# Performance work log

Hardware: AMD Instinct MI355X
Metric: run time of the kernel (lower is better)

Reference implementation:

```python
import jax, jax.numpy as jnp
import numpy as np

B, C, N, T = 16, 32, 1024, 64
C_OUT = 32
ORDER = 2
SMOOTH_DEPTH = 1


def setup_inputs() -> dict:
    key = jax.random.key(0)
    k1, k2, k3, k4 = jax.random.split(key, 4)
    x = jax.random.normal(k1, (B, C, N, T), dtype=jnp.float32)
    # row-normalized dense adjacencies (transition matrices), as used in Graph-WaveNet-style supports
    AL = jax.random.uniform(k2, (N, N), dtype=jnp.float32)
    AL = AL / AL.sum(axis=-1, keepdims=True)
    AS_pos = jax.random.uniform(k3, (N, N), dtype=jnp.float32)
    AS_pos = AS_pos / AS_pos.sum(axis=-1, keepdims=True)
    # 1x1 conv mlp: in_channels = (order*support_len+1)*c_in = 3*C, out_channels = C_OUT
    W_mlp = jax.random.normal(k4, (C_OUT, (ORDER + 1) * C), dtype=jnp.float32) * 0.02
    b_mlp = jnp.zeros((C_OUT,), dtype=jnp.float32)
    return {"x": x, "AL": AL, "AS_pos": AS_pos, "W_mlp": W_mlp, "b_mlp": b_mlp}


def reference(x, AL, AS_pos, W_mlp, b_mlp):
    # gcn_module.forward with short_bool=True, smooth_depth=SMOOTH_DEPTH, eval mode (no dropout)
    ALp = jnp.linalg.matrix_power(AL, SMOOTH_DEPTH)          # [N,N]
    # torch.einsum('bckj,ik->bcij', x, ALp): contract node dim of x against ALp
    x_long = jnp.einsum('ik,bckt->bcit', ALp, x)             # [B,C,N,T]
    x_short = x - x_long
    outs = [x]
    for _ in range(ORDER):
        # dnconv: einsum('nvw,ncwl->ncvl', A, x) with 2D A broadcast over batch
        x_long = jnp.einsum('vw,bcwt->bcvt', AL, x_long)
        x_short = jnp.einsum('vw,bcwt->bcvt', AS_pos, x_short)
        outs.append(x_long + x_short)
    h = jnp.concatenate(outs, axis=1)                        # [B,(ORDER+1)*C,N,T]
    # 1x1 conv == channel mixing
    h = jnp.einsum('oc,bcnt->bont', W_mlp, h) + b_mlp[None, :, None, None]
    return h
```

## Files before the change

kernel.cpp:

```cpp
#include <hip/hip_runtime.h>


typedef __bf16 bf16x8 __attribute__((ext_vector_type(8)));
typedef float f32x4 __attribute__((ext_vector_type(4)));
typedef unsigned int u32x4 __attribute__((ext_vector_type(4)));
typedef unsigned int u32x2 __attribute__((ext_vector_type(2)));

__device__ __forceinline__ unsigned short f2bf(float f) {
  unsigned u = __builtin_bit_cast(unsigned, f);
  u += 0x7fffu + ((u >> 16) & 1u);
  return (unsigned short)(u >> 16);
}
__device__ __forceinline__ float bf2f(unsigned short h) {
  unsigned u = ((unsigned)h) << 16;
  return __builtin_bit_cast(float, u);
}

static constexpr size_t OFF_YC    = 0;
static constexpr size_t OFF_ALBF  = 201326592;
static constexpr size_t OFF_ALT   = OFF_ALBF  + 2097152;
static constexpr size_t OFF_ASBF  = OFF_ALT   + 2097152;
static constexpr size_t OFF_AST   = OFF_ASBF  + 2097152;
static constexpr size_t OFF_AL2   = OFF_AST   + 2097152;
static constexpr size_t OFF_AL2T  = OFF_AL2   + 2097152;
static constexpr size_t OFF_ASAL  = OFF_AL2T  + 2097152;
static constexpr size_t OFF_AS2   = OFF_ASAL  + 2097152;
static constexpr size_t OFF_AL3   = OFF_AS2   + 2097152;
static constexpr size_t OFF_AS2AL = OFF_AL3   + 2097152;
static constexpr size_t OFF_G     = OFF_AS2AL + 2097152;

__global__ __launch_bounds__(256) void k_prep(const float* __restrict__ AL,
                                              const float* __restrict__ AS,
                                              unsigned short* __restrict__ ALn,
                                              unsigned short* __restrict__ ALtr,
                                              unsigned short* __restrict__ ASn,
                                              unsigned short* __restrict__ AStr) {
  const float* src = blockIdx.z ? AS : AL;
  unsigned short* dstN = blockIdx.z ? ASn : ALn;
  unsigned short* dstT = blockIdx.z ? AStr : ALtr;
  __shared__ float Xs[64][65];
  const int tid = threadIdx.x;
  const int r0 = blockIdx.x * 64, c0 = blockIdx.y * 64;
  const int lrow = tid >> 4, lc4 = tid & 15;
#pragma unroll
  for (int rr = 0; rr < 4; rr++) {
    int row = rr * 16 + lrow;
    float4 v = *(const float4*)(src + (size_t)(r0 + row) * 1024 + c0 + lc4 * 4);
    Xs[row][lc4 * 4 + 0] = v.x;
    Xs[row][lc4 * 4 + 1] = v.y;
    Xs[row][lc4 * 4 + 2] = v.z;
    Xs[row][lc4 * 4 + 3] = v.w;
    unsigned lo = (unsigned)f2bf(v.x) | ((unsigned)f2bf(v.y) << 16);
    unsigned hi = (unsigned)f2bf(v.z) | ((unsigned)f2bf(v.w) << 16);
    u32x2 pk = {lo, hi};
    *(u32x2*)(dstN + (size_t)(r0 + row) * 1024 + c0 + lc4 * 4) = pk;
  }
  __syncthreads();
  const int wc = tid & 7;
#pragma unroll
  for (int u = 0; u < 2; u++) {
    int t = u * 32 + (tid >> 3);
    unsigned v0 = (unsigned)f2bf(Xs[wc * 8 + 0][t]) | ((unsigned)f2bf(Xs[wc * 8 + 1][t]) << 16);
    unsigned v1 = (unsigned)f2bf(Xs[wc * 8 + 2][t]) | ((unsigned)f2bf(Xs[wc * 8 + 3][t]) << 16);
    unsigned v2 = (unsigned)f2bf(Xs[wc * 8 + 4][t]) | ((unsigned)f2bf(Xs[wc * 8 + 5][t]) << 16);
    unsigned v3 = (unsigned)f2bf(Xs[wc * 8 + 6][t]) | ((unsigned)f2bf(Xs[wc * 8 + 7][t]) << 16);
    u32x4 pk = {v0, v1, v2, v3};
    *(u32x4*)(dstT + (size_t)(c0 + t) * 1024 + r0 + wc * 8) = pk;
  }
}

__device__ __forceinline__ void gemm128_bt(const unsigned short* __restrict__ A,
                                           const unsigned short* __restrict__ Bt,
                                           unsigned short* __restrict__ Cp,
                                           int K, size_t ldc, int m0, int n0) {
  __shared__ unsigned short As[128 * 32];
  __shared__ unsigned short Bs[128 * 32];
  const int tid = threadIdx.x;
  const int wave = tid >> 6, lane = tid & 63;
  const int lane15 = lane & 15, quad = lane >> 4;
  const int wm = wave & 1, wn = wave >> 1;
  const int srow = lane >> 2;
  const int schunk = (lane & 3) * 8;

  const unsigned short* gA0 = A + (size_t)(m0 + wave * 16 + srow) * K + schunk;
  const unsigned short* gA1 = A + (size_t)(m0 + 64 + wave * 16 + srow) * K + schunk;
  const unsigned short* gB0 = Bt + (size_t)(n0 + wave * 16 + srow) * K + schunk;
  const unsigned short* gB1 = Bt + (size_t)(n0 + 64 + wave * 16 + srow) * K + schunk;
  unsigned short* lA0 = As + (wave * 16) * 32;
  unsigned short* lA1 = As + (64 + wave * 16) * 32;
  unsigned short* lB0 = Bs + (wave * 16) * 32;
  unsigned short* lB1 = Bs + (64 + wave * 16) * 32;

  f32x4 acc[4][4];
#pragma unroll
  for (int i = 0; i < 4; i++)
#pragma unroll
    for (int j = 0; j < 4; j++) acc[i][j] = (f32x4){0.f, 0.f, 0.f, 0.f};

  const unsigned short* pa = As + (wm * 64 + lane15) * 32 + quad * 8;
  const unsigned short* pb = Bs + (wn * 64 + lane15) * 32 + quad * 8;

  for (int kb = 0; kb < K; kb += 32) {
    __syncthreads();
    __builtin_amdgcn_global_load_lds(
        (const __attribute__((address_space(1))) unsigned int*)(gA0 + kb),
        (__attribute__((address_space(3))) unsigned int*)lA0, 16, 0, 0);
    __builtin_amdgcn_global_load_lds(
        (const __attribute__((address_space(1))) unsigned int*)(gA1 + kb),
        (__attribute__((address_space(3))) unsigned int*)lA1, 16, 0, 0);
    __builtin_amdgcn_global_load_lds(
        (const __attribute__((address_space(1))) unsigned int*)(gB0 + kb),
        (__attribute__((address_space(3))) unsigned int*)lB0, 16, 0, 0);
    __builtin_amdgcn_global_load_lds(
        (const __attribute__((address_space(1))) unsigned int*)(gB1 + kb),
        (__attribute__((address_space(3))) unsigned int*)lB1, 16, 0, 0);
    __syncthreads();

    bf16x8 av[4], bv[4];
#pragma unroll
    for (int mt = 0; mt < 4; mt++) av[mt] = *(const bf16x8*)(pa + mt * 16 * 32);
#pragma unroll
    for (int nt = 0; nt < 4; nt++) bv[nt] = *(const bf16x8*)(pb + nt * 16 * 32);
#pragma unroll
    for (int mt = 0; mt < 4; mt++)
#pragma unroll
      for (int nt = 0; nt < 4; nt++)
        acc[mt][nt] = __builtin_amdgcn_mfma_f32_16x16x32_bf16(av[mt], bv[nt], acc[mt][nt], 0, 0, 0);
  }

#pragma unroll
  for (int mt = 0; mt < 4; mt++) {
#pragma unroll
    for (int nt = 0; nt < 4; nt++) {
      const int col = n0 + wn * 64 + nt * 16 + lane15;
#pragma unroll
      for (int r = 0; r < 4; r++) {
        const int row = m0 + wm * 64 + mt * 16 + quad * 4 + r;
        Cp[(size_t)row * ldc + col] = f2bf(acc[mt][nt][r]);
      }
    }
  }
}

__global__ __launch_bounds__(256) void k_gemm_pre(char* ws, int stage) {
  const unsigned short* A;
  const unsigned short* Bt;
  unsigned short* Cp;
  const int z = blockIdx.z;
  unsigned short* ALbf = (unsigned short*)(ws + OFF_ALBF);
  unsigned short* ALt  = (unsigned short*)(ws + OFF_ALT);
  unsigned short* ASbf = (unsigned short*)(ws + OFF_ASBF);
  unsigned short* ASt  = (unsigned short*)(ws + OFF_AST);
  unsigned short* AL2  = (unsigned short*)(ws + OFF_AL2);
  unsigned short* ASAL = (unsigned short*)(ws + OFF_ASAL);
  unsigned short* AS2  = (unsigned short*)(ws + OFF_AS2);
  unsigned short* AL3  = (unsigned short*)(ws + OFF_AL3);
  unsigned short* AS2AL= (unsigned short*)(ws + OFF_AS2AL);
  if (stage == 0) {
    if (z == 0)      { A = ALbf; Bt = ALt;  Cp = AL2;  }
    else if (z == 1) { A = ASbf; Bt = ALt;  Cp = ASAL; }
    else             { A = ASbf; Bt = ASt;  Cp = AS2;  }
  } else {
    if (z == 0)      { A = AL2;  Bt = ALt;  Cp = AL3;  }
    else             { A = AS2;  Bt = ALt;  Cp = AS2AL;}
  }
  gemm128_bt(A, Bt, Cp, 1024, 1024, blockIdx.y * 128, blockIdx.x * 128);
}

__global__ __launch_bounds__(256) void k_assemble_G(const unsigned short* __restrict__ AL2,
                                                    const unsigned short* __restrict__ ASAL,
                                                    const float* __restrict__ ASf,
                                                    const unsigned short* __restrict__ AL3,
                                                    const unsigned short* __restrict__ AS2,
                                                    const unsigned short* __restrict__ AS2AL,
                                                    const float* __restrict__ W,
                                                    unsigned short* __restrict__ Wall,
                                                    unsigned short* __restrict__ G) {
  if (blockIdx.x == 0) {
    for (int k = threadIdx.x; k < 3072; k += 256) {
      int oo = k >> 5, c = k & 31;
      Wall[k] = f2bf(W[(oo & 31) * 96 + (oo >> 5) * 32 + c]);
    }
  }
  int i = blockIdx.x * 256 + threadIdx.x;
  int r = i >> 10, c = i & 1023;
  float g1 = bf2f(AL2[i]) + ASf[i] - bf2f(ASAL[i]);
  float g2 = bf2f(AL3[i]) + bf2f(AS2[i]) - bf2f(AS2AL[i]);
  G[(size_t)r * 2048 + c]        = f2bf(g1);
  G[(size_t)r * 2048 + 1024 + c] = f2bf(g2);
}

__global__ __launch_bounds__(256, 8) void k_mix_g(const float* __restrict__ x,
                                                  const unsigned short* __restrict__ Wall,
                                                  unsigned short* __restrict__ Yc) {
  const int tid = threadIdx.x;
  const int sid = (blockIdx.x & 7) * 256 + (blockIdx.x >> 3);
  const int b   = sid >> 7;
  const int n8g = sid & 127;
  const int nbase = n8g * 8;
  const int wave = tid >> 6, lane = tid & 63;
  const int lane15 = lane & 15, quad = lane >> 4;
  const int t = wave * 16 + lane15;

  bf16x8 afr[6];
#pragma unroll
  for (int ot = 0; ot < 6; ot++)
    afr[ot] = *(const bf16x8*)(Wall + (ot * 16 + lane15) * 32 + quad * 8);

  const float* xb = x + (size_t)b * 2097152 + (size_t)(quad * 8) * 65536 + t;

  bf16x8 bfr[8];
#pragma unroll
  for (int nl = 0; nl < 8; nl++) {
    const float* xp = xb + (size_t)(nbase + nl) * 64;
    unsigned u[4];
#pragma unroll
    for (int e = 0; e < 4; e++) {
      float a  = xp[(size_t)(2 * e) * 65536];
      float c2 = xp[(size_t)(2 * e + 1) * 65536];
      u[e] = (unsigned)f2bf(a) | ((unsigned)f2bf(c2) << 16);
    }
    u32x4 pk = {u[0], u[1], u[2], u[3]};
    bfr[nl] = __builtin_bit_cast(bf16x8, pk);
  }

#pragma unroll
  for (int ot = 0; ot < 6; ot++) {
    f32x4 acc[8];
    const f32x4 z = (f32x4){0.f, 0.f, 0.f, 0.f};
#pragma unroll
    for (int nl = 0; nl < 8; nl++)
      acc[nl] = __builtin_amdgcn_mfma_f32_16x16x32_bf16(afr[ot], bfr[nl], z, 0, 0, 0);
    const int og = ot >> 1;
    const int o  = (ot & 1) * 16 + quad * 4;
    const size_t plane = (size_t)(og * 128 + n8g) * 262144;
#pragma unroll
    for (int r = 0; r < 4; r++) {
      unsigned u0 = (unsigned)f2bf(acc[0][r]) | ((unsigned)f2bf(acc[1][r]) << 16);
      unsigned u1 = (unsigned)f2bf(acc[2][r]) | ((unsigned)f2bf(acc[3][r]) << 16);
      unsigned u2 = (unsigned)f2bf(acc[4][r]) | ((unsigned)f2bf(acc[5][r]) << 16);
      unsigned u3 = (unsigned)f2bf(acc[6][r]) | ((unsigned)f2bf(acc[7][r]) << 16);
      u32x4 pk = {u0, u1, u2, u3};
      size_t j = (size_t)(b * 32 + o + r) * 64 + t;
      *(u32x4*)(Yc + plane + j * 8) = pk;
    }
  }
}

__global__ __launch_bounds__(512) void k_gemm_main8(const unsigned short* __restrict__ A,
                                                    const unsigned short* __restrict__ Yc,
                                                    const float* __restrict__ bm,
                                                    float* __restrict__ out) {
  __shared__ unsigned short lds[65536];
  const int tid = threadIdx.x;
  const int wave = tid >> 6, lane = tid & 63;
  const int lane15 = lane & 15, quad = lane >> 4;
  const int wr = wave >> 2, wc = wave & 3;

  const int bid = blockIdx.x;
  const int swz = (bid & 7) * 64 + (bid >> 3);
  const int nx = swz >> 2, my = swz & 3;
  const int m0 = my * 256, n0 = nx * 256;

  const int srow = tid >> 3;
  const int cB   = (tid & 7) ^ (srow & 7);
  const int skc  = cB << 3;
  const int ldst0 = (tid & ~63) << 3;

#define STAGE_A(rowbase, ldsptr, ktile)                                                 \
  do {                                                                                  \
    const unsigned short* _g =                                                          \
        A + (size_t)((rowbase) + srow) * 2048 + (size_t)((ktile) * 64 + skc);           \
    __builtin_amdgcn_global_load_lds(                                                   \
        (const __attribute__((address_space(1))) unsigned int*)_g,                      \
        (__attribute__((address_space(3))) unsigned int*)((ldsptr) + ldst0), 16, 0, 0); \
    __builtin_amdgcn_global_load_lds(                                                   \
        (const __attribute__((address_space(1))) unsigned int*)(_g + 131072),           \
        (__attribute__((address_space(3))) unsigned int*)((ldsptr) + 4096 + ldst0),     \
        16, 0, 0);                                                                      \
  } while (0)

#define STAGE_B(rowbase, ldsptr, ktile)                                                 \
  do {                                                                                  \
    const unsigned short* _g = Yc + (size_t)(128 + (ktile) * 8 + cB) * 262144 +         \
                               (size_t)((rowbase) + srow) * 8;                          \
    __builtin_amdgcn_global_load_lds(                                                   \
        (const __attribute__((address_space(1))) unsigned int*)_g,                      \
        (__attribute__((address_space(3))) unsigned int*)((ldsptr) + ldst0), 16, 0, 0); \
    __builtin_amdgcn_global_load_lds(                                                   \
        (const __attribute__((address_space(1))) unsigned int*)(_g + 512),              \
        (__attribute__((address_space(3))) unsigned int*)((ldsptr) + 4096 + ldst0),     \
        16, 0, 0);                                                                      \
  } while (0)

#define RD_BFR()                                                                        \
  _Pragma("unroll") for (int n = 0; n < 4; n++)                                         \
      _Pragma("unroll") for (int kk = 0; kk < 2; kk++)                                  \
          bfr[n][kk] = *(const bf16x8*)(pB + n * 1024 + aks[kk]);

#define RD_AFR(mA, mB)                                                                  \
  _Pragma("unroll") for (int kk = 0; kk < 2; kk++) {                                    \
    afr[0][kk] = *(const bf16x8*)(pA + (mA) * 1024 + aks[kk]);                          \
    afr[1][kk] = *(const bf16x8*)(pA + (mB) * 1024 + aks[kk]);                          \
  }

#define MFMA2(i0)                                                                       \
  _Pragma("unroll") for (int kk = 0; kk < 2; kk++)                                      \
      _Pragma("unroll") for (int mi = 0; mi < 2; mi++)                                  \
          _Pragma("unroll") for (int n = 0; n < 4; n++)                                 \
              acc[(i0) + mi][n] = __builtin_amdgcn_mfma_f32_16x16x32_bf16(              \
                  afr[mi][kk], bfr[n][kk], acc[(i0) + mi][n], 0, 0, 0);

#define BAR()   asm volatile("" ::: "memory"); __builtin_amdgcn_s_barrier();
#define LGKM0() asm volatile("s_waitcnt lgkmcnt(0)" ::: "memory");                      \
                __builtin_amdgcn_sched_barrier(0);
#define LGKM8() asm volatile("s_waitcnt lgkmcnt(8)" ::: "memory");
#define PRIO1() __builtin_amdgcn_s_setprio(1);
#define PRIO0() __builtin_amdgcn_s_setprio(0);

  unsigned short* Acur = lds;
  unsigned short* Bcur = lds + 16384;
  unsigned short* Aalt = lds + 32768;
  unsigned short* Balt = lds + 49152;

  f32x4 acc[8][4];
#pragma unroll
  for (int i = 0; i < 8; i++)
#pragma unroll
    for (int j = 0; j < 4; j++) acc[i][j] = (f32x4){0.f, 0.f, 0.f, 0.f};

  const int swz8 = (lane15 & 7) << 3;
  int aks[2];
  aks[0] = (quad << 3) ^ swz8;
  aks[1] = (32 | (quad << 3)) ^ swz8;

  bf16x8 bfr[4][2], afr[2][2];

  STAGE_A(m0,       Acur,        0);
  STAGE_A(m0 + 128, Acur + 8192, 0);
  STAGE_B(n0,       Bcur,        0);
  STAGE_B(n0 + 128, Bcur + 8192, 0);
  STAGE_B(n0,       Balt,        1);
  STAGE_B(n0 + 128, Balt + 8192, 1);
  asm volatile("s_waitcnt vmcnt(4)" ::: "memory");
  BAR();

  for (int t = 0; t < 30; ++t) {
    const unsigned short* pA = Acur + (wr * 128 + lane15) * 64;
    const unsigned short* pB = Bcur + (wc * 64 + lane15) * 64;
    RD_BFR();
    RD_AFR(0, 1);
    STAGE_A(m0, Aalt, t + 1);
    LGKM8();
    BAR(); LGKM0();
    PRIO1(); MFMA2(0); PRIO0();
    BAR();
    RD_AFR(2, 3);
    STAGE_A(m0 + 128, Aalt + 8192, t + 1);
    BAR(); LGKM0();
    PRIO1(); MFMA2(2); PRIO0();
    BAR();
    RD_AFR(4, 5);
    STAGE_B(n0, Bcur, t + 2);
    BAR(); LGKM0();
    PRIO1(); MFMA2(4); PRIO0();
    BAR();
    RD_AFR(6, 7);
    STAGE_B(n0 + 128, Bcur + 8192, t + 2);
    BAR(); LGKM0();
    PRIO1(); MFMA2(6); PRIO0();
    asm volatile("s_waitcnt vmcnt(4)" ::: "memory");
    BAR();
    unsigned short* tmp;
    tmp = Acur; Acur = Aalt; Aalt = tmp;
    tmp = Bcur; Bcur = Balt; Balt = tmp;
  }

  {
    const unsigned short* pA = Acur + (wr * 128 + lane15) * 64;
    const unsigned short* pB = Bcur + (wc * 64 + lane15) * 64;
    RD_BFR();
    RD_AFR(0, 1);
    STAGE_A(m0, Aalt, 31);
    LGKM8();
    BAR(); LGKM0();
    PRIO1(); MFMA2(0); PRIO0();
    BAR();
    RD_AFR(2, 3);
    STAGE_A(m0 + 128, Aalt + 8192, 31);
    BAR(); LGKM0();
    PRIO1(); MFMA2(2); PRIO0();
    BAR();
    RD_AFR(4, 5);
    BAR(); LGKM0();
    PRIO1(); MFMA2(4); PRIO0();
    BAR();
    RD_AFR(6, 7);
    BAR(); LGKM0();
    PRIO1(); MFMA2(6); PRIO0();
    asm volatile("s_waitcnt vmcnt(0)" ::: "memory");
    BAR();
    unsigned short* tmp;
    tmp = Acur; Acur = Aalt; Aalt = tmp;
    tmp = Bcur; Bcur = Balt; Balt = tmp;
  }

  {
    const unsigned short* pA = Acur + (wr * 128 + lane15) * 64;
    const unsigned short* pB = Bcur + (wc * 64 + lane15) * 64;
    RD_BFR();
#pragma unroll
    for (int p = 0; p < 4; p++) {
      RD_AFR(2 * p, 2 * p + 1);
      LGKM0();
      MFMA2(2 * p);
    }
  }

#pragma unroll
  for (int mt = 0; mt < 8; mt++) {
    const int row = m0 + wr * 128 + mt * 16 + quad * 4;
#pragma unroll
    for (int nf = 0; nf < 4; nf++) {
      const int col = n0 + wc * 64 + nf * 16 + lane15;
      const int bo_idx = col >> 6;
      const float bo = bm[bo_idx & 31];
      const size_t obase = (size_t)bo_idx * 65536 + (col & 63);
      ushort4 yv = *(const ushort4*)(Yc + (size_t)(row >> 3) * 262144 +
                                     (size_t)col * 8 + (row & 7));
      out[obase + (size_t)(row + 0) * 64] = acc[mt][nf][0] + bf2f(yv.x) + bo;
      out[obase + (size_t)(row + 1) * 64] = acc[mt][nf][1] + bf2f(yv.y) + bo;
      out[obase + (size_t)(row + 2) * 64] = acc[mt][nf][2] + bf2f(yv.z) + bo;
      out[obase + (size_t)(row + 3) * 64] = acc[mt][nf][3] + bf2f(yv.w) + bo;
    }
  }
#undef STAGE_A
#undef STAGE_B
#undef RD_BFR
#undef RD_AFR
#undef MFMA2
#undef BAR
#undef LGKM0
#undef LGKM8
#undef PRIO1
#undef PRIO0
}

extern "C" void kernel_launch(void* const* d_in, const int* in_sizes, int n_in,
                              void* d_out, int out_size, void* d_ws, size_t ws_size,
                              hipStream_t stream) {
  const float* x  = (const float*)d_in[0];
  const float* AL = (const float*)d_in[1];
  const float* AS = (const float*)d_in[2];
  const float* W  = (const float*)d_in[3];
  const float* bm = (const float*)d_in[4];
  float* out = (float*)d_out;
  char* ws = (char*)d_ws;

  unsigned short* Yc    = (unsigned short*)(ws + OFF_YC);
  unsigned short* ALbf  = (unsigned short*)(ws + OFF_ALBF);
  unsigned short* ALt   = (unsigned short*)(ws + OFF_ALT);
  unsigned short* ASbf  = (unsigned short*)(ws + OFF_ASBF);
  unsigned short* ASt   = (unsigned short*)(ws + OFF_AST);
  unsigned short* AL2   = (unsigned short*)(ws + OFF_AL2);
  unsigned short* ASAL  = (unsigned short*)(ws + OFF_ASAL);
  unsigned short* AS2   = (unsigned short*)(ws + OFF_AS2);
  unsigned short* AL3   = (unsigned short*)(ws + OFF_AL3);
  unsigned short* AS2AL = (unsigned short*)(ws + OFF_AS2AL);
  unsigned short* Gm    = (unsigned short*)(ws + OFF_G);
  unsigned short* Wall  = (unsigned short*)(ws + OFF_ALBF);

  k_prep<<<dim3(16, 16, 2), 256, 0, stream>>>(AL, AS, ALbf, ALt, ASbf, ASt);
  k_gemm_pre<<<dim3(8, 8, 3), 256, 0, stream>>>(ws, 0);
  k_gemm_pre<<<dim3(8, 8, 2), 256, 0, stream>>>(ws, 1);
  k_assemble_G<<<4096, 256, 0, stream>>>(AL2, ASAL, AS, AL3, AS2, AS2AL, W, Wall, Gm);
  k_mix_g<<<2048, 256, 0, stream>>>(x, Wall, Yc);
  k_gemm_main8<<<dim3(512, 1, 1), 512, 0, stream>>>(Gm, Yc, bm, out);
}
```

Before: 511.2 us.

## Halve main GEMM K-tile to 32 to cut LDS and raise occupancy

```diff
diff --git a/kernel.cpp b/kernel.cpp
--- a/kernel.cpp
+++ b/kernel.cpp
@@ -247,11 +247,11 @@
   }
 }
 
-__global__ __launch_bounds__(512) void k_gemm_main8(const unsigned short* __restrict__ A,
-                                                    const unsigned short* __restrict__ Yc,
-                                                    const float* __restrict__ bm,
-                                                    float* __restrict__ out) {
-  __shared__ unsigned short lds[65536];
+__global__ __launch_bounds__(512, 4) void k_gemm_main8(const unsigned short* __restrict__ A,
+                                                       const unsigned short* __restrict__ Yc,
+                                                       const float* __restrict__ bm,
+                                                       float* __restrict__ out) {
+  __shared__ unsigned short lds[32768];
   const int tid = threadIdx.x;
   const int wave = tid >> 6, lane = tid & 63;
   const int lane15 = lane & 15, quad = lane >> 4;
@@ -262,66 +262,52 @@
   const int nx = swz >> 2, my = swz & 3;
   const int m0 = my * 256, n0 = nx * 256;
 
-  const int srow = tid >> 3;
-  const int cB   = (tid & 7) ^ (srow & 7);
-  const int skc  = cB << 3;
-  const int ldst0 = (tid & ~63) << 3;
-
-#define STAGE_A(rowbase, ldsptr, ktile)                                                 \
-  do {                                                                                  \
-    const unsigned short* _g =                                                          \
-        A + (size_t)((rowbase) + srow) * 2048 + (size_t)((ktile) * 64 + skc);           \
-    __builtin_amdgcn_global_load_lds(                                                   \
-        (const __attribute__((address_space(1))) unsigned int*)_g,                      \
-        (__attribute__((address_space(3))) unsigned int*)((ldsptr) + ldst0), 16, 0, 0); \
-    __builtin_amdgcn_global_load_lds(                                                   \
-        (const __attribute__((address_space(1))) unsigned int*)(_g + 131072),           \
-        (__attribute__((address_space(3))) unsigned int*)((ldsptr) + 4096 + ldst0),     \
-        16, 0, 0);                                                                      \
+  const int srow = tid >> 2;
+  const int cswz = (tid & 3) ^ (srow & 3);
+  const int ldst0 = tid * 8;
+
+#define STAGE_A32(rowbase, dsthalf, ktile)                                              \
+  do {                                                                                 \
+    const unsigned short* _g =                                                         \
+        A + (size_t)((rowbase) + srow) * 2048 + (size_t)((ktile) * 32 + cswz * 8);     \
+    __builtin_amdgcn_global_load_lds(                                                  \
+        (const __attribute__((address_space(1))) unsigned int*)_g,                     \
+        (__attribute__((address_space(3))) unsigned int*)((dsthalf) + ldst0), 16, 0, 0);\
   } while (0)
 
-#define STAGE_B(rowbase, ldsptr, ktile)                                                 \
-  do {                                                                                  \
-    const unsigned short* _g = Yc + (size_t)(128 + (ktile) * 8 + cB) * 262144 +         \
-                               (size_t)((rowbase) + srow) * 8;                          \
-    __builtin_amdgcn_global_load_lds(                                                   \
-        (const __attribute__((address_space(1))) unsigned int*)_g,                      \
-        (__attribute__((address_space(3))) unsigned int*)((ldsptr) + ldst0), 16, 0, 0); \
-    __builtin_amdgcn_global_load_lds(                                                   \
-        (const __attribute__((address_space(1))) unsigned int*)(_g + 512),              \
-        (__attribute__((address_space(3))) unsigned int*)((ldsptr) + 4096 + ldst0),     \
-        16, 0, 0);                                                                      \
+#define STAGE_B32(rowbase, dsthalf, ktile)                                              \
+  do {                                                                                 \
+    const unsigned short* _g = Yc + (size_t)(128 + (ktile) * 4 + cswz) * 262144 +      \
+                               (size_t)((rowbase) + srow) * 8;                         \
+    __builtin_amdgcn_global_load_lds(                                                  \
+        (const __attribute__((address_space(1))) unsigned int*)_g,                     \
+        (__attribute__((address_space(3))) unsigned int*)((dsthalf) + ldst0), 16, 0, 0);\
   } while (0)
 
-#define RD_BFR()                                                                        \
+#define RD_B32()                                                                        \
   _Pragma("unroll") for (int n = 0; n < 4; n++)                                         \
-      _Pragma("unroll") for (int kk = 0; kk < 2; kk++)                                  \
-          bfr[n][kk] = *(const bf16x8*)(pB + n * 1024 + aks[kk]);
-
-#define RD_AFR(mA, mB)                                                                  \
-  _Pragma("unroll") for (int kk = 0; kk < 2; kk++) {                                    \
-    afr[0][kk] = *(const bf16x8*)(pA + (mA) * 1024 + aks[kk]);                          \
-    afr[1][kk] = *(const bf16x8*)(pA + (mB) * 1024 + aks[kk]);                          \
-  }
-
-#define MFMA2(i0)                                                                       \
-  _Pragma("unroll") for (int kk = 0; kk < 2; kk++)                                      \
-      _Pragma("unroll") for (int mi = 0; mi < 2; mi++)                                  \
-          _Pragma("unroll") for (int n = 0; n < 4; n++)                                 \
-              acc[(i0) + mi][n] = __builtin_amdgcn_mfma_f32_16x16x32_bf16(              \
-                  afr[mi][kk], bfr[n][kk], acc[(i0) + mi][n], 0, 0, 0);
+      bfr[n] = *(const bf16x8*)(pB + n * 512 + aks);
+
+#define RD_A32(m0i)                                                                     \
+  _Pragma("unroll") for (int mi = 0; mi < 4; mi++)                                      \
+      afr[mi] = *(const bf16x8*)(pA + ((m0i) + mi) * 512 + aks);
+
+#define MFMA16(i0)                                                                      \
+  _Pragma("unroll") for (int mi = 0; mi < 4; mi++)                                      \
+      _Pragma("unroll") for (int n = 0; n < 4; n++)                                     \
+          acc[(i0) + mi][n] = __builtin_amdgcn_mfma_f32_16x16x32_bf16(                  \
+              afr[mi], bfr[n], acc[(i0) + mi][n], 0, 0, 0);
 
 #define BAR()   asm volatile("" ::: "memory"); __builtin_amdgcn_s_barrier();
 #define LGKM0() asm volatile("s_waitcnt lgkmcnt(0)" ::: "memory");                      \
                 __builtin_amdgcn_sched_barrier(0);
-#define LGKM8() asm volatile("s_waitcnt lgkmcnt(8)" ::: "memory");
 #define PRIO1() __builtin_amdgcn_s_setprio(1);
 #define PRIO0() __builtin_amdgcn_s_setprio(0);
 
   unsigned short* Acur = lds;
-  unsigned short* Bcur = lds + 16384;
-  unsigned short* Aalt = lds + 32768;
-  unsigned short* Balt = lds + 49152;
+  unsigned short* Bcur = lds + 8192;
+  unsigned short* Aalt = lds + 16384;
+  unsigned short* Balt = lds + 24576;
 
   f32x4 acc[8][4];
 #pragma unroll
@@ -329,47 +315,35 @@
 #pragma unroll
     for (int j = 0; j < 4; j++) acc[i][j] = (f32x4){0.f, 0.f, 0.f, 0.f};
 
-  const int swz8 = (lane15 & 7) << 3;
-  int aks[2];
-  aks[0] = (quad << 3) ^ swz8;
-  aks[1] = (32 | (quad << 3)) ^ swz8;
-
-  bf16x8 bfr[4][2], afr[2][2];
-
-  STAGE_A(m0,       Acur,        0);
-  STAGE_A(m0 + 128, Acur + 8192, 0);
-  STAGE_B(n0,       Bcur,        0);
-  STAGE_B(n0 + 128, Bcur + 8192, 0);
-  STAGE_B(n0,       Balt,        1);
-  STAGE_B(n0 + 128, Balt + 8192, 1);
-  asm volatile("s_waitcnt vmcnt(4)" ::: "memory");
+  const int aks = ((quad ^ (lane15 & 3)) << 3);
+
+  bf16x8 bfr[4], afr[4];
+
+  STAGE_A32(m0,       Acur,        0);
+  STAGE_A32(m0 + 128, Acur + 4096, 0);
+  STAGE_B32(n0,       Bcur,        0);
+  STAGE_B32(n0 + 128, Bcur + 4096, 0);
+  STAGE_B32(n0,       Balt,        1);
+  STAGE_B32(n0 + 128, Balt + 4096, 1);
+  asm volatile("s_waitcnt vmcnt(2)" ::: "memory");
   BAR();
 
-  for (int t = 0; t < 30; ++t) {
-    const unsigned short* pA = Acur + (wr * 128 + lane15) * 64;
-    const unsigned short* pB = Bcur + (wc * 64 + lane15) * 64;
-    RD_BFR();
-    RD_AFR(0, 1);
-    STAGE_A(m0, Aalt, t + 1);
-    LGKM8();
+  for (int t = 0; t < 62; ++t) {
+    const unsigned short* pA = Acur + wr * 4096 + lane15 * 32;
+    const unsigned short* pB = Bcur + (wc >> 1) * 4096 + ((wc & 1) * 64 + lane15) * 32;
+    RD_B32();
+    RD_A32(0);
+    STAGE_A32(m0,       Aalt,        t + 1);
+    STAGE_A32(m0 + 128, Aalt + 4096, t + 1);
     BAR(); LGKM0();
-    PRIO1(); MFMA2(0); PRIO0();
+    PRIO1(); MFMA16(0); PRIO0();
     BAR();
-    RD_AFR(2, 3);
-    STAGE_A(m0 + 128, Aalt + 8192, t + 1);
+    RD_A32(4);
+    STAGE_B32(n0,       Bcur,        t + 2);
+    STAGE_B32(n0 + 128, Bcur + 4096, t + 2);
     BAR(); LGKM0();
-    PRIO1(); MFMA2(2); PRIO0();
-    BAR();
-    RD_AFR(4, 5);
-    STAGE_B(n0, Bcur, t + 2);
-    BAR(); LGKM0();
-    PRIO1(); MFMA2(4); PRIO0();
-    BAR();
-    RD_AFR(6, 7);
-    STAGE_B(n0 + 128, Bcur + 8192, t + 2);
-    BAR(); LGKM0();
-    PRIO1(); MFMA2(6); PRIO0();
-    asm volatile("s_waitcnt vmcnt(4)" ::: "memory");
+    PRIO1(); MFMA16(4); PRIO0();
+    asm volatile("s_waitcnt vmcnt(2)" ::: "memory");
     BAR();
     unsigned short* tmp;
     tmp = Acur; Acur = Aalt; Aalt = tmp;
@@ -377,27 +351,18 @@
   }
 
   {
-    const unsigned short* pA = Acur + (wr * 128 + lane15) * 64;
-    const unsigned short* pB = Bcur + (wc * 64 + lane15) * 64;
-    RD_BFR();
-    RD_AFR(0, 1);
-    STAGE_A(m0, Aalt, 31);
-    LGKM8();
+    const unsigned short* pA = Acur + wr * 4096 + lane15 * 32;
+    const unsigned short* pB = Bcur + (wc >> 1) * 4096 + ((wc & 1) * 64 + lane15) * 32;
+    RD_B32();
+    RD_A32(0);
+    STAGE_A32(m0,       Aalt,        63);
+    STAGE_A32(m0 + 128, Aalt + 4096, 63);
     BAR(); LGKM0();
-    PRIO1(); MFMA2(0); PRIO0();
+    PRIO1(); MFMA16(0); PRIO0();
     BAR();
-    RD_AFR(2, 3);
-    STAGE_A(m0 + 128, Aalt + 8192, 31);
+    RD_A32(4);
     BAR(); LGKM0();
-    PRIO1(); MFMA2(2); PRIO0();
-    BAR();
-    RD_AFR(4, 5);
-    BAR(); LGKM0();
-    PRIO1(); MFMA2(4); PRIO0();
-    BAR();
-    RD_AFR(6, 7);
-    BAR(); LGKM0();
-    PRIO1(); MFMA2(6); PRIO0();
+    PRIO1(); MFMA16(4); PRIO0();
     asm volatile("s_waitcnt vmcnt(0)" ::: "memory");
     BAR();
     unsigned short* tmp;
@@ -406,15 +371,15 @@
   }
 
   {
-    const unsigned short* pA = Acur + (wr * 128 + lane15) * 64;
-    const unsigned short* pB = Bcur + (wc * 64 + lane15) * 64;
-    RD_BFR();
-#pragma unroll
-    for (int p = 0; p < 4; p++) {
-      RD_AFR(2 * p, 2 * p + 1);
-      LGKM0();
-      MFMA2(2 * p);
-    }
+    const unsigned short* pA = Acur + wr * 4096 + lane15 * 32;
+    const unsigned short* pB = Bcur + (wc >> 1) * 4096 + ((wc & 1) * 64 + lane15) * 32;
+    RD_B32();
+    RD_A32(0);
+    LGKM0();
+    MFMA16(0);
+    RD_A32(4);
+    LGKM0();
+    MFMA16(4);
   }
 
 #pragma unroll
@@ -434,14 +399,13 @@
       out[obase + (size_t)(row + 3) * 64] = acc[mt][nf][3] + bf2f(yv.w) + bo;
     }
   }
-#undef STAGE_A
-#undef STAGE_B
-#undef RD_BFR
-#undef RD_AFR
-#undef MFMA2
+#undef STAGE_A32
+#undef STAGE_B32
+#undef RD_B32
+#undef RD_A32
+#undef MFMA16
 #undef BAR
 #undef LGKM0
-#undef LGKM8
 #undef PRIO1
 #undef PRIO0
 }
```

Result: slower. 1.526 ms (+198.6%).
